# Kernel optimization log

Measured on AMD Instinct MI355X. Metric: run time of the kernel, lower is better.

The kernel has to match this reference:

```python
import jax, jax.numpy as jnp
import numpy as np
import math

B, SQ, SK = 8, 1024, 1024
DIM_Q = DIM_K = DIM_V = 512
H = 8
EPS = 1e-5
INF = jnp.float32(1e38)


def _ln(x, g, b):
    mu = jnp.mean(x, axis=-1, keepdims=True)
    var = jnp.mean(jnp.square(x - mu), axis=-1, keepdims=True)
    return (x - mu) * jax.lax.rsqrt(var + EPS) * g + b


def setup_inputs() -> dict:
    key = jax.random.key(0)
    ks = jax.random.split(key, 12)
    s = 1.0 / math.sqrt(DIM_V)
    return {
        "queries": jax.random.normal(ks[0], (B, SQ, DIM_Q), jnp.float32),
        "keys": jax.random.normal(ks[1], (B, SK, DIM_K), jnp.float32),
        # binary presence masks (as in the original usage)
        "presence_q": (jax.random.uniform(ks[2], (B, SQ)) > 0.1).astype(jnp.float32),
        "presence_k": (jax.random.uniform(ks[3], (B, SK)) > 0.1).astype(jnp.float32),
        "num_heads": H,
        "Wq": jax.random.normal(ks[4], (DIM_Q, DIM_V), jnp.float32) * s,
        "bq": jnp.zeros((DIM_V,), jnp.float32),
        "Wk": jax.random.normal(ks[5], (DIM_K, DIM_V), jnp.float32) * s,
        "bk": jnp.zeros((DIM_V,), jnp.float32),
        "Wv": jax.random.normal(ks[6], (DIM_K, DIM_V), jnp.float32) * s,
        "bv": jnp.zeros((DIM_V,), jnp.float32),
        "Wo": jax.random.normal(ks[7], (DIM_V, DIM_V), jnp.float32) * s,
        "bo": jnp.zeros((DIM_V,), jnp.float32),
        "g0": jnp.ones((DIM_V,), jnp.float32),
        "b0": jnp.zeros((DIM_V,), jnp.float32),
        "g1": jnp.ones((DIM_V,), jnp.float32),
        "b1": jnp.zeros((DIM_V,), jnp.float32),
    }


def reference(queries, keys, presence_q, presence_k, num_heads,
              Wq, bq, Wk, bk, Wv, bv, Wo, bo, g0, b0, g1, b1):
    b, sq, _ = queries.shape
    dim_v = Wq.shape[1]
    d = dim_v // num_heads
    q = queries @ Wq + bq                              # [B,Sq,V]
    k = keys @ Wk + bk                                 # [B,Sk,V]
    v = keys @ Wv + bv                                 # [B,Sk,V]
    qh = q.reshape(b, sq, num_heads, d)
    kh = k.reshape(b, -1, num_heads, d)
    vh = v.reshape(b, -1, num_heads, d)
    logits = jnp.einsum('bqhd,bkhd->bhqk', qh, kh) / jnp.float32(math.sqrt(dim_v))
    pq = presence_q[:, None, :, None]                  # [B,1,Sq,1]
    logits = pq * logits - (1.0 - pq) * INF
    pk = presence_k[:, None, None, :]                  # [B,1,1,Sk]
    logits = pk * logits - (1.0 - pk) * INF
    A = jax.nn.softmax(logits, axis=-1)                # [B,H,Sq,Sk]
    o = qh + jnp.einsum('bhqk,bkhd->bqhd', A, vh)      # residual add of Q_
    o = o.reshape(b, sq, dim_v)
    o = _ln(o, g0, b0)
    o = o + jax.nn.relu(o @ Wo + bo)
    o = _ln(o, g1, b1)
    return o
```

## Files before the change

### kernel.cpp

```cpp
#include <hip/hip_runtime.h>

typedef __attribute__((ext_vector_type(8))) short short8;
typedef __attribute__((ext_vector_type(4))) float f32x4;

#define SCALE2 0.06375871571f

__device__ __forceinline__ float bfu(unsigned short u){
  return __uint_as_float(((unsigned int)u) << 16);
}
__device__ __forceinline__ unsigned short f2b(float x){
  unsigned int b = __float_as_uint(x);
  return (unsigned short)((b + 0x7fffu + ((b>>16)&1u)) >> 16);
}
__device__ __forceinline__ uint4 pack8(const float* f){
  float4 a = *(const float4*)f, b = *(const float4*)(f+4);
  uint4 r;
  r.x = (unsigned)f2b(a.x) | ((unsigned)f2b(a.y)<<16);
  r.y = (unsigned)f2b(a.z) | ((unsigned)f2b(a.w)<<16);
  r.z = (unsigned)f2b(b.x) | ((unsigned)f2b(b.y)<<16);
  r.w = (unsigned)f2b(b.z) | ((unsigned)f2b(b.w)<<16);
  return r;
}

__global__ __launch_bounds__(256) void prep_inputs(
    const float* Wq, const float* Wk, const float* Wv, const float* Wo,
    const float* q, const float* k, unsigned short* wt, unsigned short* qk_dst)
{
  const int id = blockIdx.x, t = threadIdx.x;
  if (id < 256){
    const int m = id >> 6;
    const float* W = (m==0)?Wq:(m==1)?Wk:(m==2)?Wv:Wo;
    unsigned short* dst = wt + (long)m*262144;
    __shared__ unsigned short tile[64][72];
    const int n0 = ((id>>3)&7)*64, k0 = (id&7)*64;
    {
      int r = t>>2, c0 = (t&3)*16;
      uint4 u0 = pack8(W + (long)(k0+r)*512 + n0 + c0);
      uint4 u1 = pack8(W + (long)(k0+r)*512 + n0 + c0 + 8);
      unsigned short* us0 = (unsigned short*)&u0;
      unsigned short* us1 = (unsigned short*)&u1;
      #pragma unroll
      for (int i=0;i<8;++i) tile[c0+i][r] = us0[i];
      #pragma unroll
      for (int i=0;i<8;++i) tile[c0+8+i][r] = us1[i];
    }
    __syncthreads();
    {
      int n = t>>2, ks = (t&3)*16;
      *(uint4*)(dst + (long)(n0+n)*512 + k0 + ks)     = *(uint4*)&tile[n][ks];
      *(uint4*)(dst + (long)(n0+n)*512 + k0 + ks + 8) = *(uint4*)&tile[n][ks+8];
    }
  } else {
    long i = ((long)(id-256)*256 + t)*8;
    const float* src = (i < 4194304) ? q + i : k + (i - 4194304);
    *(uint4*)(qk_dst + i) = pack8(src);
  }
}

__global__ __launch_bounds__(256) void proj_mfma(
    const unsigned short* qin, const unsigned short* kin, const unsigned short* wt,
    const float* bq, const float* bk, const float* bv,
    unsigned short* q_bf, unsigned short* k_bf, unsigned short* vt_bf)
{
  const int mat = blockIdx.z;
  const unsigned short* A = (mat==0)? qin : kin;
  const unsigned short* Wt = wt + (long)mat*262144;
  const float* bias = (mat==0)?bq:(mat==1)?bk:bv;
  const int row0 = blockIdx.y*128, col0 = blockIdx.x*128;
  __shared__ unsigned short As[2][128][40];
  __shared__ unsigned short Ws[2][128][40];
  const int t = threadIdx.x;
  const int lane = t & 63, wid = t >> 6;
  const int ln = lane & 15, quad = lane >> 4;
  const int wy = wid >> 1, wx = wid & 1;
  f32x4 acc[4][4];
  #pragma unroll
  for (int i=0;i<4;++i){
    #pragma unroll
    for (int j=0;j<4;++j) acc[i][j] = (f32x4){0.f,0.f,0.f,0.f};
  }
  const int sr = t>>1, sk0 = (t&1)*16;
  const unsigned short* Arow = A  + (long)(row0+sr)*512 + sk0;
  const unsigned short* Wrow = Wt + (long)(col0+sr)*512 + sk0;
  uint4 a0 = *(const uint4*)(Arow);
  uint4 a1 = *(const uint4*)(Arow + 8);
  uint4 w0 = *(const uint4*)(Wrow);
  uint4 w1 = *(const uint4*)(Wrow + 8);
  *(uint4*)&As[0][sr][sk0]   = a0;
  *(uint4*)&As[0][sr][sk0+8] = a1;
  *(uint4*)&Ws[0][sr][sk0]   = w0;
  *(uint4*)&Ws[0][sr][sk0+8] = w1;
  __syncthreads();
  for (int it=0; it<16; ++it){
    const int cur = it & 1;
    if (it < 15){
      a0 = *(const uint4*)(Arow + (it+1)*32);
      a1 = *(const uint4*)(Arow + (it+1)*32 + 8);
      w0 = *(const uint4*)(Wrow + (it+1)*32);
      w1 = *(const uint4*)(Wrow + (it+1)*32 + 8);
    }
    short8 a[4], b[4];
    #pragma unroll
    for (int mt=0;mt<4;++mt) a[mt] = *(const short8*)&As[cur][wy*64+mt*16+ln][quad*8];
    #pragma unroll
    for (int nt=0;nt<4;++nt) b[nt] = *(const short8*)&Ws[cur][wx*64+nt*16+ln][quad*8];
    #pragma unroll
    for (int mt=0;mt<4;++mt){
      #pragma unroll
      for (int nt=0;nt<4;++nt)
        acc[mt][nt] = __builtin_amdgcn_mfma_f32_16x16x32_bf16(a[mt], b[nt], acc[mt][nt], 0,0,0);
    }
    if (it < 15){
      *(uint4*)&As[cur^1][sr][sk0]   = a0;
      *(uint4*)&As[cur^1][sr][sk0+8] = a1;
      *(uint4*)&Ws[cur^1][sr][sk0]   = w0;
      *(uint4*)&Ws[cur^1][sr][sk0+8] = w1;
    }
    __syncthreads();
  }
  float bias_v[4];
  #pragma unroll
  for (int nt=0;nt<4;++nt) bias_v[nt] = bias[col0 + wx*64 + nt*16 + ln];
  if (mat < 2){
    unsigned short* dst = (mat==0)? q_bf : k_bf;
    #pragma unroll
    for (int mt=0;mt<4;++mt){
      int row = row0 + wy*64 + mt*16 + quad*4;
      #pragma unroll
      for (int nt=0;nt<4;++nt){
        int col = col0 + wx*64 + nt*16 + ln;
        #pragma unroll
        for (int r=0;r<4;++r)
          dst[(long)(row+r)*512 + col] = f2b(acc[mt][nt][r] + bias_v[nt]);
      }
    }
  } else {
    #pragma unroll
    for (int mt=0;mt<4;++mt){
      int row = row0 + wy*64 + mt*16 + quad*4;
      int bb = row >> 10, sk = row & 1023;
      #pragma unroll
      for (int nt=0;nt<4;++nt){
        int col = col0 + wx*64 + nt*16 + ln;
        int h = col >> 6, dd = col & 63;
        uint2 pk2; unsigned short* pp = (unsigned short*)&pk2;
        #pragma unroll
        for (int r=0;r<4;++r) pp[r] = f2b(acc[mt][nt][r] + bias_v[nt]);
        *(uint2*)(vt_bf + (((long)((bb*8+h)*64+dd)) << 10) + sk) = pk2;
      }
    }
  }
}

__global__ __launch_bounds__(256, 3) void attn_mfma(
    const unsigned short* q_bf, const unsigned short* k_bf, const unsigned short* vt_bf,
    const float* pres_q, const float* pres_k, unsigned short* o_bf)
{
  const int bx = blockIdx.x;
  const int b = bx >> 3, h = bx & 7;
  const int q0 = blockIdx.y * 64;
  const int t = threadIdx.x;
  const int lane = t & 63, wid = t >> 6, ln = lane & 15, quad = lane >> 4;
  __shared__ unsigned short Ks[2][64][72];
  __shared__ unsigned short Vt[2][64][72];
  __shared__ unsigned short Pw[4][16][72];
  __shared__ float pk_s[2][64];
  {
    int tok = t>>2, ds = (t&3)*16;
    const unsigned short* sk = k_bf + (long)(b*1024 + tok)*512 + h*64 + ds;
    *(uint4*)&Ks[0][tok][ds]   = *(const uint4*)sk;
    *(uint4*)&Ks[0][tok][ds+8] = *(const uint4*)(sk+8);
    const unsigned short* sv = vt_bf + (((long)((b*8+h)*64 + tok)) << 10) + ds;
    *(uint4*)&Vt[0][tok][ds]   = *(const uint4*)sv;
    *(uint4*)&Vt[0][tok][ds+8] = *(const uint4*)(sv+8);
  }
  if (t < 64) pk_s[0][t] = pres_k[b*1024 + t];
  const unsigned short* qrow = q_bf + (long)(b*1024 + q0 + wid*16 + ln)*512 + h*64;
  short8 aq0 = *(const short8*)(qrow + quad*8);
  short8 aq1 = *(const short8*)(qrow + 32 + quad*8);
  const float av = SCALE2 * pres_q[b*1024 + q0 + wid*16 + ln];
  const float mval = (av == 0.f) ? 0.f : -43.f;
  f32x4 oacc[4];
  #pragma unroll
  for (int i=0;i<4;++i) oacc[i] = (f32x4){0.f,0.f,0.f,0.f};
  float lsum = 0.f;
  __syncthreads();

  for (int it=0; it<16; ++it){
    const int cur = it & 1;
    const int k0n = (it+1)*64;
    uint4 pf_k0, pf_k1, pf_v0, pf_v1; float pf_p = 0.f;
    if (it < 15){
      int tok = t>>2, ds = (t&3)*16;
      const unsigned short* sk = k_bf + (long)(b*1024 + k0n + tok)*512 + h*64 + ds;
      pf_k0 = *(const uint4*)sk;
      pf_k1 = *(const uint4*)(sk+8);
      const unsigned short* sv = vt_bf + (((long)((b*8+h)*64 + tok)) << 10) + k0n + ds;
      pf_v0 = *(const uint4*)sv;
      pf_v1 = *(const uint4*)(sv+8);
      if (t < 64) pf_p = pres_k[b*1024 + k0n + t];
    }
    f32x4 sc[4];
    #pragma unroll
    for (int kt=0;kt<4;++kt) sc[kt] = (f32x4){0.f,0.f,0.f,0.f};
    __builtin_amdgcn_s_setprio(1);
    #pragma unroll
    for (int kt=0;kt<4;++kt){
      short8 kb0 = *(const short8*)&Ks[cur][kt*16+ln][quad*8];
      short8 kb1 = *(const short8*)&Ks[cur][kt*16+ln][32+quad*8];
      sc[kt] = __builtin_amdgcn_mfma_f32_16x16x32_bf16(kb0, aq0, sc[kt], 0,0,0);
      sc[kt] = __builtin_amdgcn_mfma_f32_16x16x32_bf16(kb1, aq1, sc[kt], 0,0,0);
    }
    __builtin_amdgcn_s_setprio(0);
    #pragma unroll
    for (int kt=0;kt<4;++kt){
      float4 pk4 = *(const float4*)&pk_s[cur][kt*16 + quad*4];
      float x0 = __builtin_fmaf(pk4.x, __builtin_fmaf(sc[kt][0], av, -mval), mval);
      float x1 = __builtin_fmaf(pk4.y, __builtin_fmaf(sc[kt][1], av, -mval), mval);
      float x2 = __builtin_fmaf(pk4.z, __builtin_fmaf(sc[kt][2], av, -mval), mval);
      float x3 = __builtin_fmaf(pk4.w, __builtin_fmaf(sc[kt][3], av, -mval), mval);
      float e0 = __builtin_amdgcn_exp2f(x0);
      float e1 = __builtin_amdgcn_exp2f(x1);
      float e2 = __builtin_amdgcn_exp2f(x2);
      float e3 = __builtin_amdgcn_exp2f(x3);
      lsum += (e0+e1)+(e2+e3);
      uint2 w;
      w.x = (unsigned)f2b(e0) | ((unsigned)f2b(e1)<<16);
      w.y = (unsigned)f2b(e2) | ((unsigned)f2b(e3)<<16);
      *(uint2*)&Pw[wid][ln][kt*16 + quad*4] = w;
    }
    short8 ap0 = *(const short8*)&Pw[wid][ln][quad*8];
    short8 ap1 = *(const short8*)&Pw[wid][ln][32 + quad*8];
    __builtin_amdgcn_s_setprio(1);
    #pragma unroll
    for (int dt=0;dt<4;++dt){
      short8 vb0 = *(const short8*)&Vt[cur][dt*16+ln][quad*8];
      short8 vb1 = *(const short8*)&Vt[cur][dt*16+ln][32+quad*8];
      oacc[dt] = __builtin_amdgcn_mfma_f32_16x16x32_bf16(ap0, vb0, oacc[dt], 0,0,0);
      oacc[dt] = __builtin_amdgcn_mfma_f32_16x16x32_bf16(ap1, vb1, oacc[dt], 0,0,0);
    }
    __builtin_amdgcn_s_setprio(0);
    if (it < 15){
      int tok = t>>2, ds = (t&3)*16;
      *(uint4*)&Ks[cur^1][tok][ds]   = pf_k0;
      *(uint4*)&Ks[cur^1][tok][ds+8] = pf_k1;
      *(uint4*)&Vt[cur^1][tok][ds]   = pf_v0;
      *(uint4*)&Vt[cur^1][tok][ds+8] = pf_v1;
      if (t < 64) pk_s[cur^1][t] = pf_p;
    }
    __syncthreads();
  }
  float l = lsum;
  l += __shfl_xor(l, 16);
  l += __shfl_xor(l, 32);
  #pragma unroll
  for (int r=0;r<4;++r){
    float lr = __shfl(l, quad*4 + r);
    float inv = 1.f / lr;
    int ql = wid*16 + quad*4 + r;
    long base = (long)(b*1024 + q0 + ql)*512 + h*64;
    #pragma unroll
    for (int dt=0;dt<4;++dt){
      float qh = bfu(q_bf[base + dt*16 + ln]);
      o_bf[base + dt*16 + ln] = f2b(qh + oacc[dt][r]*inv);
    }
  }
}

__global__ __launch_bounds__(256) void ln_kernel(
    const unsigned short* in, void* outp, int mode, const float* g, const float* bvec)
{
  const int row = blockIdx.x*4 + (threadIdx.x >> 6);
  const int lane = threadIdx.x & 63;
  uint4 raw = *(const uint4*)(in + (long)row*512 + lane*8);
  const unsigned short* rs16 = (const unsigned short*)&raw;
  float v[8];
  #pragma unroll
  for (int c=0;c<8;++c) v[c] = bfu(rs16[c]);
  float sum = 0.f;
  #pragma unroll
  for (int c=0;c<8;++c) sum += v[c];
  #pragma unroll
  for (int msk=1; msk<64; msk<<=1) sum += __shfl_xor(sum, msk);
  float mu = sum * (1.f/512.f);
  float var = 0.f;
  #pragma unroll
  for (int c=0;c<8;++c){ v[c] -= mu; var += v[c]*v[c]; }
  #pragma unroll
  for (int msk=1; msk<64; msk<<=1) var += __shfl_xor(var, msk);
  float rs = rsqrtf(var*(1.f/512.f) + 1e-5f);
  float gv[8], bv[8];
  *(float4*)&gv[0] = *(const float4*)(g + lane*8);
  *(float4*)&gv[4] = *(const float4*)(g + lane*8 + 4);
  *(float4*)&bv[0] = *(const float4*)(bvec + lane*8);
  *(float4*)&bv[4] = *(const float4*)(bvec + lane*8 + 4);
  float y[8];
  #pragma unroll
  for (int c=0;c<8;++c) y[c] = v[c]*rs*gv[c] + bv[c];
  if (mode){
    float* dst = (float*)outp + (long)row*512 + lane*8;
    *(float4*)dst       = *(float4*)&y[0];
    *(float4*)(dst + 4) = *(float4*)&y[4];
  } else {
    uint4 out; unsigned short* os = (unsigned short*)&out;
    #pragma unroll
    for (int c=0;c<8;++c) os[c] = f2b(y[c]);
    *(uint4*)((unsigned short*)outp + (long)row*512 + lane*8) = out;
  }
}

__global__ __launch_bounds__(256) void out_mfma(
    const unsigned short* t_bf, const unsigned short* Wt, const float* bo,
    unsigned short* u_bf)
{
  const int row0 = blockIdx.y*64, col0 = blockIdx.x*128;
  __shared__ unsigned short As[2][64][40];
  __shared__ unsigned short Ws[2][128][40];
  const int t = threadIdx.x;
  const int lane = t & 63, wid = t >> 6;
  const int ln = lane & 15, quad = lane >> 4;
  const int wy = wid >> 1, wx = wid & 1;
  f32x4 acc[2][4];
  #pragma unroll
  for (int i=0;i<2;++i){
    #pragma unroll
    for (int j=0;j<4;++j) acc[i][j] = (f32x4){0.f,0.f,0.f,0.f};
  }
  const int ar = t>>2, ac0 = (t&3)*8;
  const int wr = t>>1, wc0 = (t&1)*16;
  const unsigned short* Arow = t_bf + (long)(row0+ar)*512 + ac0;
  const unsigned short* Wrow = Wt   + (long)(col0+wr)*512 + wc0;
  uint4 a0 = *(const uint4*)(Arow);
  uint4 w0 = *(const uint4*)(Wrow);
  uint4 w1 = *(const uint4*)(Wrow + 8);
  *(uint4*)&As[0][ar][ac0] = a0;
  *(uint4*)&Ws[0][wr][wc0]   = w0;
  *(uint4*)&Ws[0][wr][wc0+8] = w1;
  __syncthreads();
  for (int it=0; it<16; ++it){
    const int cur = it & 1;
    if (it < 15){
      a0 = *(const uint4*)(Arow + (it+1)*32);
      w0 = *(const uint4*)(Wrow + (it+1)*32);
      w1 = *(const uint4*)(Wrow + (it+1)*32 + 8);
    }
    short8 a[2], b[4];
    #pragma unroll
    for (int mt=0;mt<2;++mt) a[mt] = *(const short8*)&As[cur][wy*32+mt*16+ln][quad*8];
    #pragma unroll
    for (int nt=0;nt<4;++nt) b[nt] = *(const short8*)&Ws[cur][wx*64+nt*16+ln][quad*8];
    #pragma unroll
    for (int mt=0;mt<2;++mt){
      #pragma unroll
      for (int nt=0;nt<4;++nt)
        acc[mt][nt] = __builtin_amdgcn_mfma_f32_16x16x32_bf16(a[mt], b[nt], acc[mt][nt], 0,0,0);
    }
    if (it < 15){
      *(uint4*)&As[cur^1][ar][ac0] = a0;
      *(uint4*)&Ws[cur^1][wr][wc0]   = w0;
      *(uint4*)&Ws[cur^1][wr][wc0+8] = w1;
    }
    __syncthreads();
  }
  float bias_v[4];
  #pragma unroll
  for (int nt=0;nt<4;++nt) bias_v[nt] = bo[col0 + wx*64 + nt*16 + ln];
  #pragma unroll
  for (int mt=0;mt<2;++mt){
    int row = row0 + wy*32 + mt*16 + quad*4;
    #pragma unroll
    for (int nt=0;nt<4;++nt){
      int col = col0 + wx*64 + nt*16 + ln;
      #pragma unroll
      for (int r=0;r<4;++r){
        long idx = (long)(row+r)*512 + col;
        float u = acc[mt][nt][r] + bias_v[nt];
        u = fmaxf(u, 0.f);
        u_bf[idx] = f2b(bfu(t_bf[idx]) + u);
      }
    }
  }
}

extern "C" void kernel_launch(void* const* d_in, const int* in_sizes, int n_in,
                              void* d_out, int out_size, void* d_ws, size_t ws_size,
                              hipStream_t stream)
{
  unsigned short* q_bf  = (unsigned short*)d_ws;
  unsigned short* k_bf  = q_bf  + 8192l*512;
  unsigned short* vt_bf = k_bf  + 8192l*512;
  unsigned short* t_bf  = vt_bf + 8192l*512;
  unsigned short* wt    = t_bf  + 8192l*512;
  unsigned short* qin   = wt + 4l*512*512;
  unsigned short* kin   = qin + 4194304;
  unsigned short* o_bf  = qin;
  unsigned short* u_bf  = kin;

  hipLaunchKernelGGL(prep_inputs, dim3(4352), dim3(256), 0, stream,
                     (const float*)d_in[5], (const float*)d_in[7],
                     (const float*)d_in[9], (const float*)d_in[11],
                     (const float*)d_in[0], (const float*)d_in[1], wt, qin);
  hipLaunchKernelGGL(proj_mfma, dim3(4,64,3), dim3(256), 0, stream,
                     qin, kin, wt,
                     (const float*)d_in[6], (const float*)d_in[8],
                     (const float*)d_in[10], q_bf, k_bf, vt_bf);
  hipLaunchKernelGGL(attn_mfma, dim3(64,16), dim3(256), 0, stream,
                     q_bf, k_bf, vt_bf,
                     (const float*)d_in[2], (const float*)d_in[3], o_bf);
  hipLaunchKernelGGL(ln_kernel, dim3(2048), dim3(256), 0, stream,
                     o_bf, (void*)t_bf, 0, (const float*)d_in[13], (const float*)d_in[14]);
  hipLaunchKernelGGL(out_mfma, dim3(4,128), dim3(256), 0, stream,
                     t_bf, wt + 3l*512*512, (const float*)d_in[12], u_bf);
  hipLaunchKernelGGL(ln_kernel, dim3(2048), dim3(256), 0, stream,
                     u_bf, d_out, 1, (const float*)d_in[15], (const float*)d_in[16]);
}
```

Baseline: 214.0 us.

## Load K/V fragments directly to registers and process two query tiles per wave

The attention kernel no longer stages K and V through shared memory with double buffering and block barriers. Each wave now loads its MFMA operand fragments for K and V straight from global memory into registers, and software-prefetches the next K tile. Each wave also handles 32 query rows instead of 16, so every K/V fragment is reused across two query subtiles, and the grid is halved to match. The cost is higher register pressure (launch bounds drop from 3 to 2 blocks), and every wave now issues its own redundant global loads of K and V, which the caches must absorb.

```diff
diff --git a/kernel.cpp b/kernel.cpp
--- a/kernel.cpp
+++ b/kernel.cpp
@@ -152,117 +152,132 @@
   }
 }
 
-__global__ __launch_bounds__(256, 3) void attn_mfma(
+__global__ __launch_bounds__(256, 2) void attn_mfma(
     const unsigned short* q_bf, const unsigned short* k_bf, const unsigned short* vt_bf,
     const float* pres_q, const float* pres_k, unsigned short* o_bf)
 {
   const int bx = blockIdx.x;
   const int b = bx >> 3, h = bx & 7;
-  const int q0 = blockIdx.y * 64;
+  const int q0 = blockIdx.y * 128;
   const int t = threadIdx.x;
   const int lane = t & 63, wid = t >> 6, ln = lane & 15, quad = lane >> 4;
-  __shared__ unsigned short Ks[2][64][72];
-  __shared__ unsigned short Vt[2][64][72];
-  __shared__ unsigned short Pw[4][16][72];
-  __shared__ float pk_s[2][64];
-  {
-    int tok = t>>2, ds = (t&3)*16;
-    const unsigned short* sk = k_bf + (long)(b*1024 + tok)*512 + h*64 + ds;
-    *(uint4*)&Ks[0][tok][ds]   = *(const uint4*)sk;
-    *(uint4*)&Ks[0][tok][ds+8] = *(const uint4*)(sk+8);
-    const unsigned short* sv = vt_bf + (((long)((b*8+h)*64 + tok)) << 10) + ds;
-    *(uint4*)&Vt[0][tok][ds]   = *(const uint4*)sv;
-    *(uint4*)&Vt[0][tok][ds+8] = *(const uint4*)(sv+8);
-  }
-  if (t < 64) pk_s[0][t] = pres_k[b*1024 + t];
-  const unsigned short* qrow = q_bf + (long)(b*1024 + q0 + wid*16 + ln)*512 + h*64;
-  short8 aq0 = *(const short8*)(qrow + quad*8);
-  short8 aq1 = *(const short8*)(qrow + 32 + quad*8);
-  const float av = SCALE2 * pres_q[b*1024 + q0 + wid*16 + ln];
-  const float mval = (av == 0.f) ? 0.f : -43.f;
-  f32x4 oacc[4];
-  #pragma unroll
-  for (int i=0;i<4;++i) oacc[i] = (f32x4){0.f,0.f,0.f,0.f};
-  float lsum = 0.f;
-  __syncthreads();
+  __shared__ unsigned short Pw[4][32][72];
+
+  const unsigned short* Kb  = k_bf  + ((long)b*1024)*512 + h*64;
+  const unsigned short* Vb  = vt_bf + (((long)(b*8+h)) << 16);
+  const float* pkb = pres_k + b*1024;
+
+  short8 aq[2][2];
+  float av[2], mval[2];
+  #pragma unroll
+  for (int st=0;st<2;++st){
+    int qi = q0 + wid*32 + st*16 + ln;
+    const unsigned short* qrow = q_bf + ((long)(b*1024 + qi))*512 + h*64;
+    aq[st][0] = *(const short8*)(qrow + quad*8);
+    aq[st][1] = *(const short8*)(qrow + 32 + quad*8);
+    av[st]   = SCALE2 * pres_q[b*1024 + qi];
+    mval[st] = (av[st] == 0.f) ? 0.f : -43.f;
+  }
+  f32x4 oacc[2][4];
+  #pragma unroll
+  for (int st=0;st<2;++st){
+    #pragma unroll
+    for (int i=0;i<4;++i) oacc[st][i] = (f32x4){0.f,0.f,0.f,0.f};
+  }
+  float lsum[2] = {0.f, 0.f};
+
+  short8 kf0[4], kf1[4];
+  #pragma unroll
+  for (int kt=0;kt<4;++kt){
+    const unsigned short* kp = Kb + ((long)(kt*16+ln))*512 + quad*8;
+    kf0[kt] = *(const short8*)kp;
+    kf1[kt] = *(const short8*)(kp+32);
+  }
 
   for (int it=0; it<16; ++it){
-    const int cur = it & 1;
-    const int k0n = (it+1)*64;
-    uint4 pf_k0, pf_k1, pf_v0, pf_v1; float pf_p = 0.f;
-    if (it < 15){
-      int tok = t>>2, ds = (t&3)*16;
-      const unsigned short* sk = k_bf + (long)(b*1024 + k0n + tok)*512 + h*64 + ds;
-      pf_k0 = *(const uint4*)sk;
-      pf_k1 = *(const uint4*)(sk+8);
-      const unsigned short* sv = vt_bf + (((long)((b*8+h)*64 + tok)) << 10) + k0n + ds;
-      pf_v0 = *(const uint4*)sv;
-      pf_v1 = *(const uint4*)(sv+8);
-      if (t < 64) pf_p = pres_k[b*1024 + k0n + t];
-    }
-    f32x4 sc[4];
-    #pragma unroll
-    for (int kt=0;kt<4;++kt) sc[kt] = (f32x4){0.f,0.f,0.f,0.f};
-    __builtin_amdgcn_s_setprio(1);
-    #pragma unroll
-    for (int kt=0;kt<4;++kt){
-      short8 kb0 = *(const short8*)&Ks[cur][kt*16+ln][quad*8];
-      short8 kb1 = *(const short8*)&Ks[cur][kt*16+ln][32+quad*8];
-      sc[kt] = __builtin_amdgcn_mfma_f32_16x16x32_bf16(kb0, aq0, sc[kt], 0,0,0);
-      sc[kt] = __builtin_amdgcn_mfma_f32_16x16x32_bf16(kb1, aq1, sc[kt], 0,0,0);
-    }
-    __builtin_amdgcn_s_setprio(0);
-    #pragma unroll
-    for (int kt=0;kt<4;++kt){
-      float4 pk4 = *(const float4*)&pk_s[cur][kt*16 + quad*4];
-      float x0 = __builtin_fmaf(pk4.x, __builtin_fmaf(sc[kt][0], av, -mval), mval);
-      float x1 = __builtin_fmaf(pk4.y, __builtin_fmaf(sc[kt][1], av, -mval), mval);
-      float x2 = __builtin_fmaf(pk4.z, __builtin_fmaf(sc[kt][2], av, -mval), mval);
-      float x3 = __builtin_fmaf(pk4.w, __builtin_fmaf(sc[kt][3], av, -mval), mval);
-      float e0 = __builtin_amdgcn_exp2f(x0);
-      float e1 = __builtin_amdgcn_exp2f(x1);
-      float e2 = __builtin_amdgcn_exp2f(x2);
-      float e3 = __builtin_amdgcn_exp2f(x3);
-      lsum += (e0+e1)+(e2+e3);
-      uint2 w;
-      w.x = (unsigned)f2b(e0) | ((unsigned)f2b(e1)<<16);
-      w.y = (unsigned)f2b(e2) | ((unsigned)f2b(e3)<<16);
-      *(uint2*)&Pw[wid][ln][kt*16 + quad*4] = w;
-    }
-    short8 ap0 = *(const short8*)&Pw[wid][ln][quad*8];
-    short8 ap1 = *(const short8*)&Pw[wid][ln][32 + quad*8];
-    __builtin_amdgcn_s_setprio(1);
+    const int k0 = it*64;
+    short8 vf0[4], vf1[4];
     #pragma unroll
     for (int dt=0;dt<4;++dt){
-      short8 vb0 = *(const short8*)&Vt[cur][dt*16+ln][quad*8];
-      short8 vb1 = *(const short8*)&Vt[cur][dt*16+ln][32+quad*8];
-      oacc[dt] = __builtin_amdgcn_mfma_f32_16x16x32_bf16(ap0, vb0, oacc[dt], 0,0,0);
-      oacc[dt] = __builtin_amdgcn_mfma_f32_16x16x32_bf16(ap1, vb1, oacc[dt], 0,0,0);
-    }
-    __builtin_amdgcn_s_setprio(0);
-    if (it < 15){
-      int tok = t>>2, ds = (t&3)*16;
-      *(uint4*)&Ks[cur^1][tok][ds]   = pf_k0;
-      *(uint4*)&Ks[cur^1][tok][ds+8] = pf_k1;
-      *(uint4*)&Vt[cur^1][tok][ds]   = pf_v0;
-      *(uint4*)&Vt[cur^1][tok][ds+8] = pf_v1;
-      if (t < 64) pk_s[cur^1][t] = pf_p;
-    }
-    __syncthreads();
-  }
-  float l = lsum;
-  l += __shfl_xor(l, 16);
-  l += __shfl_xor(l, 32);
-  #pragma unroll
-  for (int r=0;r<4;++r){
-    float lr = __shfl(l, quad*4 + r);
-    float inv = 1.f / lr;
-    int ql = wid*16 + quad*4 + r;
-    long base = (long)(b*1024 + q0 + ql)*512 + h*64;
-    #pragma unroll
-    for (int dt=0;dt<4;++dt){
-      float qh = bfu(q_bf[base + dt*16 + ln]);
-      o_bf[base + dt*16 + ln] = f2b(qh + oacc[dt][r]*inv);
+      const unsigned short* vp = Vb + (((long)(dt*16+ln)) << 10) + k0 + quad*8;
+      vf0[dt] = *(const short8*)vp;
+      vf1[dt] = *(const short8*)(vp+32);
+    }
+    float4 pk4[4];
+    #pragma unroll
+    for (int kt=0;kt<4;++kt)
+      pk4[kt] = *(const float4*)(pkb + k0 + kt*16 + quad*4);
+    short8 nk0[4], nk1[4];
+    if (it < 15){
+      #pragma unroll
+      for (int kt=0;kt<4;++kt){
+        const unsigned short* kp = Kb + ((long)(k0+64+kt*16+ln))*512 + quad*8;
+        nk0[kt] = *(const short8*)kp;
+        nk1[kt] = *(const short8*)(kp+32);
+      }
+    }
+    #pragma unroll
+    for (int st=0;st<2;++st){
+      f32x4 sc[4];
+      #pragma unroll
+      for (int kt=0;kt<4;++kt) sc[kt] = (f32x4){0.f,0.f,0.f,0.f};
+      __builtin_amdgcn_s_setprio(1);
+      #pragma unroll
+      for (int kt=0;kt<4;++kt){
+        sc[kt] = __builtin_amdgcn_mfma_f32_16x16x32_bf16(kf0[kt], aq[st][0], sc[kt], 0,0,0);
+        sc[kt] = __builtin_amdgcn_mfma_f32_16x16x32_bf16(kf1[kt], aq[st][1], sc[kt], 0,0,0);
+      }
+      __builtin_amdgcn_s_setprio(0);
+      #pragma unroll
+      for (int kt=0;kt<4;++kt){
+        float x0 = __builtin_fmaf(pk4[kt].x, __builtin_fmaf(sc[kt][0], av[st], -mval[st]), mval[st]);
+        float x1 = __builtin_fmaf(pk4[kt].y, __builtin_fmaf(sc[kt][1], av[st], -mval[st]), mval[st]);
+        float x2 = __builtin_fmaf(pk4[kt].z, __builtin_fmaf(sc[kt][2], av[st], -mval[st]), mval[st]);
+        float x3 = __builtin_fmaf(pk4[kt].w, __builtin_fmaf(sc[kt][3], av[st], -mval[st]), mval[st]);
+        float e0 = __builtin_amdgcn_exp2f(x0);
+        float e1 = __builtin_amdgcn_exp2f(x1);
+        float e2 = __builtin_amdgcn_exp2f(x2);
+        float e3 = __builtin_amdgcn_exp2f(x3);
+        lsum[st] += (e0+e1)+(e2+e3);
+        uint2 w;
+        w.x = (unsigned)f2b(e0) | ((unsigned)f2b(e1)<<16);
+        w.y = (unsigned)f2b(e2) | ((unsigned)f2b(e3)<<16);
+        *(uint2*)&Pw[wid][st*16+ln][kt*16 + quad*4] = w;
+      }
+    }
+    #pragma unroll
+    for (int st=0;st<2;++st){
+      short8 ap0 = *(const short8*)&Pw[wid][st*16+ln][quad*8];
+      short8 ap1 = *(const short8*)&Pw[wid][st*16+ln][32 + quad*8];
+      __builtin_amdgcn_s_setprio(1);
+      #pragma unroll
+      for (int dt=0;dt<4;++dt){
+        oacc[st][dt] = __builtin_amdgcn_mfma_f32_16x16x32_bf16(ap0, vf0[dt], oacc[st][dt], 0,0,0);
+        oacc[st][dt] = __builtin_amdgcn_mfma_f32_16x16x32_bf16(ap1, vf1[dt], oacc[st][dt], 0,0,0);
+      }
+      __builtin_amdgcn_s_setprio(0);
+    }
+    if (it < 15){
+      #pragma unroll
+      for (int kt=0;kt<4;++kt){ kf0[kt] = nk0[kt]; kf1[kt] = nk1[kt]; }
+    }
+  }
+  #pragma unroll
+  for (int st=0;st<2;++st){
+    float l = lsum[st];
+    l += __shfl_xor(l, 16);
+    l += __shfl_xor(l, 32);
+    #pragma unroll
+    for (int r=0;r<4;++r){
+      float lr = __shfl(l, quad*4 + r);
+      float inv = 1.f / lr;
+      int ql = q0 + wid*32 + st*16 + quad*4 + r;
+      long base = ((long)(b*1024 + ql))*512 + h*64;
+      #pragma unroll
+      for (int dt=0;dt<4;++dt){
+        float qh = bfu(q_bf[base + dt*16 + ln]);
+        o_bf[base + dt*16 + ln] = f2b(qh + oacc[st][dt][r]*inv);
+      }
     }
   }
 }
@@ -404,7 +419,7 @@
                      qin, kin, wt,
                      (const float*)d_in[6], (const float*)d_in[8],
                      (const float*)d_in[10], q_bf, k_bf, vt_bf);
-  hipLaunchKernelGGL(attn_mfma, dim3(64,16), dim3(256), 0, stream,
+  hipLaunchKernelGGL(attn_mfma, dim3(64,8), dim3(256), 0, stream,
                      q_bf, k_bf, vt_bf,
                      (const float*)d_in[2], (const float*)d_in[3], o_bf);
   hipLaunchKernelGGL(ln_kernel, dim3(2048), dim3(256), 0, stream,
```

New measurement: 242.1 us. +13.1%, slower.
